# Performance work log

Measured on AMD Instinct MI355X. Metric: run time of the kernel, lower is better.

The kernel has to match this reference:

```python
import jax, jax.numpy as jnp
import numpy as np

RESO = 32          # triplane/voxel resolution
VIT = 16           # ViT patch grid resolution
PAD = 0.1
C_TRI = 64         # triplane channels per plane
C_IMG = 1280       # image feature channels
C_IN = 128         # inner (attention) channels
C_OUT = 64
NH = 8
HD = C_IN // NH
IMG_SIZE = 224.0


def pos_enc(d_model, length):
    pos = jnp.arange(length, dtype=jnp.float32)[:, None]
    div = jnp.exp(jnp.arange(0, d_model, 2, dtype=jnp.float32) * (-np.log(10000.0) / d_model))
    pe = jnp.zeros((length, d_model), jnp.float32)
    pe = pe.at[:, 0::2].set(jnp.sin(pos * div))
    pe = pe.at[:, 1::2].set(jnp.cos(pos * div))
    return pe


def bilinear_sample(feats, gx, gy):
    # feats: [B, J, H, W, C]; gx, gy: [B, J, N] in [-1, 1]; align_corners=True
    B, J, Hh, Ww, _ = feats.shape
    ux = (gx + 1.0) * 0.5 * (Ww - 1)
    uy = (gy + 1.0) * 0.5 * (Hh - 1)
    x0 = jnp.floor(ux).astype(jnp.int32)
    y0 = jnp.floor(uy).astype(jnp.int32)
    wx = (ux - x0)[..., None]
    wy = (uy - y0)[..., None]
    x1 = jnp.clip(x0 + 1, 0, Ww - 1)
    y1 = jnp.clip(y0 + 1, 0, Hh - 1)
    x0 = jnp.clip(x0, 0, Ww - 1)
    y0 = jnp.clip(y0, 0, Hh - 1)
    bi = jnp.arange(B)[:, None, None]
    ji = jnp.arange(J)[None, :, None]
    f00 = feats[bi, ji, y0, x0]
    f01 = feats[bi, ji, y0, x1]
    f10 = feats[bi, ji, y1, x0]
    f11 = feats[bi, ji, y1, x1]
    return (f00 * (1 - wx) * (1 - wy) + f01 * wx * (1 - wy)
            + f10 * (1 - wx) * wy + f11 * wx * wy)


def forward(triplane_feat, image_feat, proj_mat, k_w, k_b, q_w, q_b, v_w, v_b,
            in_w, in_b, out_w, out_b, proj_w, proj_b):
    B, n_img = image_feat.shape[0], image_feat.shape[1]
    N = RESO ** 3
    img = image_feat[:, :, 1:, :]                        # drop CLS -> [B,J,256,C_IMG]
    image_pe = pos_enc(C_IN, VIT * VIT)[None, None]      # [1,1,256,C_IN]
    k_feat = img @ k_w.T + k_b + image_pe
    v_feat = img @ v_w.T + v_b + image_pe
    k_map = k_feat.reshape(B, n_img, VIT, VIT, C_IN)     # [B,J,H,W,C]
    v_map = v_feat.reshape(B, n_img, VIT, VIT, C_IN)

    # voxel coords -> project into each camera
    idx = jnp.arange(RESO)
    X, Y, Z = jnp.meshgrid(idx, idx, idx, indexing='ij')
    vox = jnp.stack([X, Y, Z], -1).reshape(N, 3).astype(jnp.float32)
    vox = (vox / (RESO - 1) - 0.5) * 2.0 * (1.0 + PAD + 1e-5)
    homo = jnp.concatenate([vox, jnp.ones((N, 1), jnp.float32)], -1)  # [N,4]
    pc = jnp.einsum('nk,bjik->bjni', homo, proj_mat)                   # [B,J,N,4]
    px = pc[..., 0] / pc[..., 2]
    py = pc[..., 1] / pc[..., 2]
    gx = jnp.clip((px / (IMG_SIZE - 1) - 0.5) * 2.0, -1.0, 1.0)
    gy = jnp.clip((py / (IMG_SIZE - 1) - 0.5) * 2.0, -1.0, 1.0)
    # The torch code does a 3D grid_sample whose depth coordinate lands exactly
    # on each image index (align_corners=True), so it reduces to per-image
    # bilinear sampling on the 16x16 token maps.
    k_s = bilinear_sample(k_map, gx, gy)   # [B,J,N,C_IN]
    v_s = bilinear_sample(v_map, gx, gy)

    # triplane features expanded to the voxel grid (voxel order n = x*R^2+y*R+z)
    xz, xy, yz = jnp.split(triplane_feat, 3, axis=2)     # each [B,C,R,R]
    xz_t = jnp.transpose(xz, (0, 3, 2, 1))               # [B,x,z,C]
    xy_t = jnp.transpose(xy, (0, 3, 2, 1))               # [B,x,y,C]
    yz_t = jnp.transpose(yz, (0, 3, 2, 1))               # [B,y,z,C]
    shp = (B, RESO, RESO, RESO, C_TRI)
    xz_v = jnp.broadcast_to(xz_t[:, :, None, :, :], shp)
    xy_v = jnp.broadcast_to(xy_t[:, :, :, None, :], shp)
    yz_v = jnp.broadcast_to(yz_t[:, None, :, :, :], shp)
    tri = jnp.concatenate([xz_v, xy_v, yz_v], -1).reshape(B, N, 3 * C_TRI)
    q = tri @ q_w.T + q_b + pos_enc(C_IN, N)[None]       # [B,N,C_IN]

    # per-voxel cross attention (q_len=1, kv_len=n_img); torch MHA semantics
    Wq, Wk, Wv = in_w[:C_IN], in_w[C_IN:2 * C_IN], in_w[2 * C_IN:]
    bq, bk, bv = in_b[:C_IN], in_b[C_IN:2 * C_IN], in_b[2 * C_IN:]
    qh = (q @ Wq.T + bq).reshape(B, N, NH, HD)
    k_t = jnp.transpose(k_s, (0, 2, 1, 3))               # [B,N,J,C]
    v_t = jnp.transpose(v_s, (0, 2, 1, 3))
    kh = (k_t @ Wk.T + bk).reshape(B, N, n_img, NH, HD)
    vh = (v_t @ Wv.T + bv).reshape(B, N, n_img, NH, HD)
    logits = jnp.einsum('bnhd,bnjhd->bnhj', qh, kh) / np.sqrt(HD).astype(np.float32)
    attn = jax.nn.softmax(logits, axis=-1)
    o = jnp.einsum('bnhj,bnjhd->bnhd', attn, vh).reshape(B, N, C_IN)
    o = o @ out_w.T + out_b

    # mean-pool volume back to three planes
    vol = o.reshape(B, RESO, RESO, RESO, C_IN)             # [b,x,y,z,c]
    xz_o = jnp.transpose(vol.mean(axis=2), (0, 2, 1, 3))   # [b,z,x,c]
    xy_o = jnp.transpose(vol.mean(axis=3), (0, 2, 1, 3))   # [b,y,x,c]
    yz_o = jnp.transpose(vol.mean(axis=1), (0, 2, 1, 3))   # [b,z,y,c]
    planes = jnp.concatenate([xz_o, xy_o, yz_o], axis=1)   # [B,3R,R,C_IN]
    out = planes @ proj_w.T + proj_b
    return jnp.transpose(out, (0, 3, 1, 2))                # [B,C_OUT,3R,R]


def setup_inputs() -> dict:
    key = jax.random.key(0)
    ks = jax.random.split(key, 10)
    B, J = 2, 5
    s = 0.02
    base = jnp.array([[200., 0., 112., 0.],
                      [0., 200., 112., 0.],
                      [0., 0., 1., 3.5],
                      [0., 0., 0., 1.]], jnp.float32)
    return {
        'triplane_feat': jax.random.normal(ks[0], (B, C_TRI, 3 * RESO, RESO), jnp.float32),
        'image_feat': jax.random.normal(ks[1], (B, J, VIT * VIT + 1, C_IMG), jnp.float32),
        'proj_mat': base[None, None] + 0.01 * jax.random.normal(ks[2], (B, J, 4, 4), jnp.float32),
        'valid_frames': jnp.ones((B, J), jnp.int32),
        'k_w': s * jax.random.normal(ks[3], (C_IN, C_IMG), jnp.float32), 'k_b': jnp.zeros((C_IN,), jnp.float32),
        'q_w': s * jax.random.normal(ks[4], (C_IN, 3 * C_TRI), jnp.float32), 'q_b': jnp.zeros((C_IN,), jnp.float32),
        'v_w': s * jax.random.normal(ks[5], (C_IN, C_IMG), jnp.float32), 'v_b': jnp.zeros((C_IN,), jnp.float32),
        'in_w': s * jax.random.normal(ks[6], (3 * C_IN, C_IN), jnp.float32), 'in_b': jnp.zeros((3 * C_IN,), jnp.float32),
        'out_w': s * jax.random.normal(ks[7], (C_IN, C_IN), jnp.float32), 'out_b': jnp.zeros((C_IN,), jnp.float32),
        'proj_w': s * jax.random.normal(ks[8], (C_OUT, C_IN), jnp.float32), 'proj_b': jnp.zeros((C_OUT,), jnp.float32),
    }


def reference(triplane_feat, image_feat, proj_mat, valid_frames, k_w, k_b, q_w, q_b,
              v_w, v_b, in_w, in_b, out_w, out_b, proj_w, proj_b):
    # valid_frames matches the torch forward signature but is unused in its body
    return forward(triplane_feat, image_feat, proj_mat, k_w, k_b, q_w, q_b,
                   v_w, v_b, in_w, in_b, out_w, out_b, proj_w, proj_b)
```

## Files before the change

### kernel.cpp

```cpp
#include <hip/hip_runtime.h>
#include <hip/hip_bf16.h>
#include <cstddef>

#define NVOX 32768
#define J5 5
#define KB2 1472
typedef __attribute__((ext_vector_type(8))) short s16x8;
typedef __attribute__((ext_vector_type(8))) _Float16 f16x8;
typedef __attribute__((ext_vector_type(2))) _Float16 h2t;
typedef __attribute__((ext_vector_type(4))) float f32x4;

static __device__ __forceinline__ float pe_val(int pos, int c) {
  float dv = expf((float)(c & ~1) * (-0.0719557841560639f));
  float arg = (float)pos * dv;
  return (c & 1) ? cosf(arg) : sinf(arg);
}
static __device__ __forceinline__ short f2h(float f) {
  _Float16 h = (_Float16)f;
  return *reinterpret_cast<short*>(&h);
}
static __device__ __forceinline__ float h2f(short s) {
  _Float16 h = *reinterpret_cast<_Float16*>(&s);
  return (float)h;
}
static __device__ __forceinline__ float2 cmul(float2 a, float2 b) {
  return make_float2(a.x * b.x - a.y * b.y, a.x * b.y + a.y * b.x);
}
static __device__ __forceinline__ float dot8h(f16x8 a, f16x8 b, float acc) {
#if __has_builtin(__builtin_amdgcn_fdot2)
#pragma unroll
  for (int i = 0; i < 4; i++) {
    h2t x; x[0] = a[2 * i]; x[1] = a[2 * i + 1];
    h2t y; y[0] = b[2 * i]; y[1] = b[2 * i + 1];
    acc = __builtin_amdgcn_fdot2(x, y, acc, false);
  }
#else
#pragma unroll
  for (int i = 0; i < 8; i++) acc = fmaf((float)a[i], (float)b[i], acc);
#endif
  return acc;
}

#define NB_TABS   24
#define NB_WQPE   64
#define NB_WQC    96
#define NB_WO     32
#define NB_QCB    1
#define NB_TRI2   96
#define NB_FOLDW  1280
#define NB_PETAB  128
#define NB_WIN    128
#define NB_CB     1
#define B_TABS   0
#define B_WQPE   (B_TABS + NB_TABS)
#define B_WQC    (B_WQPE + NB_WQPE)
#define B_WO     (B_WQC + NB_WQC)
#define B_QCB    (B_WO + NB_WO)
#define B_TRI2   (B_QCB + NB_QCB)
#define B_FOLDW  (B_TRI2 + NB_TRI2)
#define B_PETAB  (B_FOLDW + NB_FOLDW)
#define B_WIN    (B_PETAB + NB_PETAB)
#define B_CB     (B_WIN + NB_WIN)
#define NB_TOTAL (B_CB + NB_CB)

__global__ __launch_bounds__(256) void k_prep(
    const float* __restrict__ tp,
    const float* __restrict__ k_w, const float* __restrict__ k_b,
    const float* __restrict__ q_w, const float* __restrict__ q_b,
    const float* __restrict__ v_w, const float* __restrict__ v_b,
    const float* __restrict__ in_w, const float* __restrict__ in_b,
    const float* __restrict__ out_w, const float* __restrict__ out_b,
    const float* __restrict__ proj_w, const float* __restrict__ proj_b,
    float2* __restrict__ tabs, short* __restrict__ Wqb_s, float* __restrict__ Wo,
    float* __restrict__ qcb, float* __restrict__ obb,
    short* __restrict__ tri_tb, short* __restrict__ Wkvb2, short* __restrict__ pe_tab) {
  __shared__ short tile_s[64][65];
  const int bx = blockIdx.x, t = threadIdx.x;

  if (bx < B_WQPE) {
    int idx = bx * 256 + t;
    if (idx < 6144) {
      int tb = idx >> 11, rem = idx & 2047;
      int pos = rem >> 6, i = rem & 63;
      float dv = expf((float)(2 * i) * (-0.0719557841560639f));
      float mult = (tb == 0) ? 1024.0f : (tb == 1) ? 32.0f : 1.0f;
      float ang = (float)pos * mult * dv;
      tabs[idx] = make_float2(cosf(ang), sinf(ang));
    }
  } else if (bx < B_WQC) {
    int e = (bx - B_WQPE) * 256 + t;
    int c = e >> 7, j = e & 127;
    Wqb_s[(size_t)c * 320 + 192 + j] = f2h(in_w[(size_t)c * 128 + j]);
  } else if (bx < B_WO) {
    int e = (bx - B_WQC) * 256 + t;
    int c = e / 192, k = e % 192;
    const float* ir = in_w + (size_t)c * 128;
    float acc = 0.f;
    for (int j = 0; j < 128; j++) acc = fmaf(ir[j], q_w[(size_t)j * 192 + k], acc);
    Wqb_s[(size_t)c * 320 + k] = f2h(acc);
  } else if (bx < B_QCB) {
    int e = (bx - B_WO) * 256 + t;
    int o = e >> 7, c = e & 127;
    const float* pr = proj_w + (size_t)o * 128;
    float acc = 0.f;
    for (int j = 0; j < 128; j++) acc = fmaf(pr[j], out_w[(size_t)j * 128 + c], acc);
    Wo[e] = acc;
  } else if (bx < B_TRI2) {
    if (t < 128) {
      float acc = in_b[t];
      const float* ir = in_w + (size_t)t * 128;
      for (int j = 0; j < 128; j++) acc = fmaf(ir[j], q_b[j], acc);
      qcb[t] = acc;
    }
    if (t < 64) {
      float acc = proj_b[t];
      const float* pr = proj_w + (size_t)t * 128;
      for (int j = 0; j < 128; j++) acc = fmaf(pr[j], out_b[j], acc);
      obb[t] = acc;
    }
  } else if (bx < B_FOLDW) {
    int b3 = bx - B_TRI2;
    int segb = b3 >> 4, tile = b3 & 15;
    int b = segb / 3, seg = segb % 3;
    int cc = t >> 2, q = t & 3;
#pragma unroll
    for (int di = 0; di < 2; di++) {
      int i = tile * 2 + di;
      const float* src = tp + (((size_t)(b * 64 + cc)) * 96 + seg * 32 + i) * 32 + q * 8;
      float4 a0 = *(const float4*)src;
      float4 a1 = *(const float4*)(src + 4);
      short* dst = &tile_s[cc][di * 32 + q * 8];
      dst[0] = f2h(a0.x); dst[1] = f2h(a0.y); dst[2] = f2h(a0.z); dst[3] = f2h(a0.w);
      dst[4] = f2h(a1.x); dst[5] = f2h(a1.y); dst[6] = f2h(a1.z); dst[7] = f2h(a1.w);
    }
    __syncthreads();
    int cp = t >> 2;
    int cc0 = q * 16;
    s16x8 v0, v1;
#pragma unroll
    for (int e = 0; e < 8; e++) { v0[e] = tile_s[cc0 + e][cp]; v1[e] = tile_s[cc0 + 8 + e][cp]; }
    short* outp = tri_tb + (((size_t)(b * 3 + seg) * 1024) + tile * 64 + cp) * 64 + cc0;
    *reinterpret_cast<s16x8*>(outp) = v0;
    *reinterpret_cast<s16x8*>(outp + 8) = v1;
  } else if (bx < B_PETAB) {
    int u = (bx - B_FOLDW) * 256 + t;
    int c = u / 1280, k = u % 1280;
    const float* w = (c < 128) ? k_w : v_w;
    const float* ir = in_w + (size_t)(128 + c) * 128;
    float acc = 0.f;
    for (int j = 0; j < 128; j++) acc = fmaf(ir[j], w[(size_t)j * 1280 + k], acc);
    Wkvb2[(size_t)c * KB2 + k] = f2h(acc);
  } else if (bx < B_WIN) {
    int e = (bx - B_PETAB) * 256 + t;
    int p = e >> 7, c = e & 127;
    pe_tab[e] = f2h(pe_val(p, c));
  } else if (bx < B_CB) {
    int e = (bx - B_WIN) * 256 + t;
    int c = e >> 7, j = e & 127;
    Wkvb2[(size_t)c * KB2 + 1280 + j] = f2h(in_w[(size_t)(128 + c) * 128 + j]);
  } else {
    int c = t;
    int which = c >> 7;
    const float* bias = which ? v_b : k_b;
    const float* ir = in_w + (size_t)(128 + c) * 128;
    float acc = in_b[128 + c];
    for (int j = 0; j < 128; j++) acc = fmaf(bias[j], ir[j], acc);
    short* row = Wkvb2 + (size_t)c * KB2 + 1408;
    row[0] = f2h(acc);
    for (int k = 1; k < 64; k++) row[k] = 0;
  }
}

#define NKV 320
__global__ __launch_bounds__(256) void k_qkv(
    const float* __restrict__ img, const short* __restrict__ Wkvb2,
    const short* __restrict__ pe_tab, short* __restrict__ k2b, short* __restrict__ v2b,
    const short* __restrict__ tri_tb, const short* __restrict__ Wqb_s,
    const float* __restrict__ qcb, const float2* __restrict__ tabs,
    short* __restrict__ qh_g) {
  __shared__ __align__(16) short A_lds[64 * 64];
  __shared__ __align__(16) short B_lds[128 * 64];
  const int t = threadIdx.x;
  const int lane = t & 63, w = t >> 6;

  if (blockIdx.x < NKV) {
    const int kvid = blockIdx.x;
    const int m0 = (kvid >> 2) * 32;
    const int nb0 = (kvid & 3) * 64;
    const int wm = w & 1, wn = w >> 1;
    f32x4 acc[2];
    acc[0] = (f32x4){0.f, 0.f, 0.f, 0.f};
    acc[1] = (f32x4){0.f, 0.f, 0.f, 0.f};
    for (int ct = 0; ct < 23; ct++) {
      __syncthreads();
      {
        int r = t >> 3, g = t & 7;
        s16x8 v;
        if (ct < 20) {
          int row = m0 + r;
          int bj = row >> 8, p = row & 255;
          const float* src = img + ((size_t)(bj * 257 + 1 + p)) * 1280 + ct * 64 + g * 8;
          float4 a0 = *(const float4*)src;
          float4 a1 = *(const float4*)(src + 4);
          v[0] = f2h(a0.x); v[1] = f2h(a0.y); v[2] = f2h(a0.z); v[3] = f2h(a0.w);
          v[4] = f2h(a1.x); v[5] = f2h(a1.y); v[6] = f2h(a1.z); v[7] = f2h(a1.w);
        } else if (ct < 22) {
          int p = (m0 + r) & 255;
          v = *reinterpret_cast<const s16x8*>(pe_tab + (size_t)p * 128 + (ct - 20) * 64 + g * 8);
        } else {
          v = (s16x8){0, 0, 0, 0, 0, 0, 0, 0};
          if (g == 0) v[0] = (short)0x3C00;
        }
        *reinterpret_cast<s16x8*>(&A_lds[(r * 8 + (g ^ (r & 7))) * 8]) = v;
      }
      {
#pragma unroll
        for (int it = 0; it < 2; it++) {
          int u = it * 256 + t;
          int r2 = u >> 3, g = u & 7;
          const int4 src = *reinterpret_cast<const int4*>(
              Wkvb2 + (size_t)((kvid & 3) * 64 + r2) * KB2 + ct * 64 + g * 8);
          *reinterpret_cast<int4*>(&B_lds[(r2 * 8 + (g ^ (r2 & 7))) * 8]) = src;
        }
      }
      __syncthreads();
#pragma unroll
      for (int ks = 0; ks < 2; ks++) {
        int kb = ks * 4 + (lane >> 4);
        int arow = wm * 16 + (lane & 15);
        f16x8 a = *reinterpret_cast<const f16x8*>(&A_lds[(arow * 8 + (kb ^ (arow & 7))) * 8]);
#pragma unroll
        for (int f = 0; f < 2; f++) {
          int bcol = wn * 32 + f * 16 + (lane & 15);
          f16x8 bb = *reinterpret_cast<const f16x8*>(&B_lds[(bcol * 8 + (kb ^ (bcol & 7))) * 8]);
          acc[f] = __builtin_amdgcn_mfma_f32_16x16x32_f16(a, bb, acc[f], 0, 0, 0);
        }
      }
    }
#pragma unroll
    for (int f = 0; f < 2; f++) {
#pragma unroll
      for (int reg = 0; reg < 4; reg++) {
        int grow = m0 + wm * 16 + (lane >> 4) * 4 + reg;
        int gcol = nb0 + wn * 32 + f * 16 + (lane & 15);
        int which = gcol >> 7, c = gcol & 127;
        short* dst = which ? v2b : k2b;
        dst[(size_t)grow * 128 + c] = f2h(acc[f][reg]);
      }
    }
  } else {
    const int qid = blockIdx.x - NKV;
    const int b = qid >> 9;
    const int n0 = (qid & 511) * 64;
    const int xq = n0 >> 10, yq0 = (n0 >> 5) & 31;
    const float2* tabX = tabs;
    const float2* tabY = tabs + 2048;
    const float2* tabZ = tabs + 4096;
    f32x4 acc[4][2];
#pragma unroll
    for (int m = 0; m < 4; m++)
#pragma unroll
      for (int f = 0; f < 2; f++) acc[m][f] = (f32x4){0.f, 0.f, 0.f, 0.f};

    for (int ct = 0; ct < 5; ct++) {
      __syncthreads();
      {
#pragma unroll
        for (int it = 0; it < 2; it++) {
          int u = it * 256 + t;
          int r = u >> 3, g = u & 7;
          if (ct < 3) {
            int n = n0 + r;
            int x = n >> 10, y = (n >> 5) & 31, z = n & 31;
            int cell = (ct == 0) ? (z * 32 + x) : (ct == 1) ? (y * 32 + x) : (z * 32 + y);
            const int4 src = *reinterpret_cast<const int4*>(
                tri_tb + ((size_t)(b * 3 + ct) * 1024 + cell) * 64 + g * 8);
            *reinterpret_cast<int4*>(&A_lds[(r * 8 + (g ^ (r & 7))) * 8]) = src;
          } else {
            int i0 = (ct - 3) * 32 + g * 4;
            int z = r & 31, y = yq0 + (r >> 5);
            s16x8 v;
#pragma unroll
            for (int q = 0; q < 4; q++) {
              int i = i0 + q;
              float2 exy = cmul(tabX[xq * 64 + i], tabY[y * 64 + i]);
              float2 e = cmul(exy, tabZ[z * 64 + i]);
              v[q * 2]     = f2h(e.y);
              v[q * 2 + 1] = f2h(e.x);
            }
            *reinterpret_cast<s16x8*>(&A_lds[(r * 8 + (g ^ (r & 7))) * 8]) = v;
          }
        }
      }
      {
#pragma unroll
        for (int it = 0; it < 4; it++) {
          int u = it * 256 + t;
          int col = u >> 3, g = u & 7;
          const int4 src = *reinterpret_cast<const int4*>(
              Wqb_s + (size_t)col * 320 + ct * 64 + g * 8);
          *reinterpret_cast<int4*>(&B_lds[(col * 8 + (g ^ (col & 7))) * 8]) = src;
        }
      }
      __syncthreads();
#pragma unroll
      for (int ks = 0; ks < 2; ks++) {
        int kb = ks * 4 + (lane >> 4);
        f16x8 a[4], bb[2];
#pragma unroll
        for (int m = 0; m < 4; m++) {
          int row = m * 16 + (lane & 15);
          a[m] = *reinterpret_cast<const f16x8*>(&A_lds[(row * 8 + (kb ^ (row & 7))) * 8]);
        }
#pragma unroll
        for (int f = 0; f < 2; f++) {
          int col = w * 32 + f * 16 + (lane & 15);
          bb[f] = *reinterpret_cast<const f16x8*>(&B_lds[(col * 8 + (kb ^ (col & 7))) * 8]);
        }
#pragma unroll
        for (int m = 0; m < 4; m++)
#pragma unroll
          for (int f = 0; f < 2; f++)
            acc[m][f] = __builtin_amdgcn_mfma_f32_16x16x32_f16(a[m], bb[f], acc[m][f], 0, 0, 0);
      }
    }
#pragma unroll
    for (int m = 0; m < 4; m++)
#pragma unroll
      for (int f = 0; f < 2; f++)
#pragma unroll
        for (int reg = 0; reg < 4; reg++) {
          int row = m * 16 + (lane >> 4) * 4 + reg;
          int col = w * 32 + f * 16 + (lane & 15);
          qh_g[((size_t)b * NVOX + n0 + row) * 128 + col] = f2h(acc[m][f][reg] + qcb[col]);
        }
  }
}

__global__ __launch_bounds__(256) void k_attn(
    const short* __restrict__ qh_g, const short* __restrict__ k2b,
    const short* __restrict__ v2b, const float* __restrict__ proj,
    short* __restrict__ obuf, float* __restrict__ pacc) {
  __shared__ __align__(16) ushort sIr[160][4];
  __shared__ __align__(16) float sW4[160][4];
  __shared__ __align__(16) float lg[160 * 8];
  __shared__ __align__(16) short o_lds[32][128];
  __shared__ float sxy[2][128];
  const int b = blockIdx.y;
  const int n0 = blockIdx.x * 32;
  const int t = threadIdx.x;

  if (t < 160) {
    int r = t / J5, j = t % J5;
    int n = n0 + r;
    int x = n >> 10, y = (n >> 5) & 31, z = n & 31;
    const float SC = (float)(1.0 + 0.1 + 1e-05);
    float fx = ((float)x / 31.0f - 0.5f) * 2.0f * SC;
    float fy = ((float)y / 31.0f - 0.5f) * 2.0f * SC;
    float fz = ((float)z / 31.0f - 0.5f) * 2.0f * SC;
    const float* P = proj + (size_t)(b * J5 + j) * 16;
    float pc0 = fmaf(fx, P[0], fmaf(fy, P[1], fmaf(fz, P[2],  P[3])));
    float pc1 = fmaf(fx, P[4], fmaf(fy, P[5], fmaf(fz, P[6],  P[7])));
    float pc2 = fmaf(fx, P[8], fmaf(fy, P[9], fmaf(fz, P[10], P[11])));
    float px = pc0 / pc2, py = pc1 / pc2;
    float gx = fminf(fmaxf((px / 223.0f - 0.5f) * 2.0f, -1.0f), 1.0f);
    float gy = fminf(fmaxf((py / 223.0f - 0.5f) * 2.0f, -1.0f), 1.0f);
    float ux = (gx + 1.0f) * 0.5f * 15.0f;
    float uy = (gy + 1.0f) * 0.5f * 15.0f;
    float fx0 = floorf(ux), fy0 = floorf(uy);
    int x0 = (int)fx0, y0 = (int)fy0;
    float wx = ux - fx0, wy = uy - fy0;
    int x1 = min(x0 + 1, 15), y1 = min(y0 + 1, 15);
    x0 = min(max(x0, 0), 15); y0 = min(max(y0, 0), 15);
    int rowb = (b * J5 + j) * 256;
    sIr[t][0] = (ushort)(rowb + y0 * 16 + x0);
    sIr[t][1] = (ushort)(rowb + y0 * 16 + x1);
    sIr[t][2] = (ushort)(rowb + y1 * 16 + x0);
    sIr[t][3] = (ushort)(rowb + y1 * 16 + x1);
    sW4[t][0] = (1.f - wx) * (1.f - wy);
    sW4[t][1] = wx * (1.f - wy);
    sW4[t][2] = (1.f - wx) * wy;
    sW4[t][3] = wx * wy;
  }
  __syncthreads();

  {
    const int oct = t & 15, rjIdx = t >> 4;
    const int c0 = oct * 8;
#pragma unroll
    for (int it = 0; it < 10; it++) {
      int rj = rjIdx + it * 16;
      int r = rj / J5;
      ushort4 I4 = *reinterpret_cast<const ushort4*>(sIr[rj]);
      float4 W4 = *reinterpret_cast<const float4*>(sW4[rj]);
      f16x8 t0 = *reinterpret_cast<const f16x8*>(k2b + (size_t)I4.x * 128 + c0);
      f16x8 t1 = *reinterpret_cast<const f16x8*>(k2b + (size_t)I4.y * 128 + c0);
      f16x8 t2 = *reinterpret_cast<const f16x8*>(k2b + (size_t)I4.z * 128 + c0);
      f16x8 t3 = *reinterpret_cast<const f16x8*>(k2b + (size_t)I4.w * 128 + c0);
      f16x8 q8 = *reinterpret_cast<const f16x8*>(qh_g + ((size_t)b * NVOX + n0 + r) * 128 + c0);
      float d0 = dot8h(q8, t0, 0.f);
      float d1 = dot8h(q8, t1, 0.f);
      float d2 = dot8h(q8, t2, 0.f);
      float d3 = dot8h(q8, t3, 0.f);
      float pv = fmaf(W4.x, d0, fmaf(W4.y, d1, fmaf(W4.z, d2, W4.w * d3)));
      pv += __shfl_xor(pv, 1);
      if (!(oct & 1)) lg[rj * 8 + (oct >> 1)] = pv * 0.25f;
    }
  }
  __syncthreads();

  {
    int r = t >> 3, h = t & 7;
    float l[J5];
    float m = -1e30f;
#pragma unroll
    for (int j = 0; j < J5; j++) { l[j] = lg[(r * J5 + j) * 8 + h]; m = fmaxf(m, l[j]); }
    float sden = 0.f;
#pragma unroll
    for (int j = 0; j < J5; j++) { l[j] = expf(l[j] - m); sden += l[j]; }
    float inv = 1.0f / sden;
#pragma unroll
    for (int j = 0; j < J5; j++) lg[(r * J5 + j) * 8 + h] = l[j] * inv;
  }
  __syncthreads();

  {
    const int oct = t & 15;
    const int c0 = oct * 8;
#pragma unroll
    for (int it = 0; it < 2; it++) {
      int r = (t >> 4) + it * 16;
      float o8[8] = {0.f, 0.f, 0.f, 0.f, 0.f, 0.f, 0.f, 0.f};
#pragma unroll
      for (int j = 0; j < J5; j++) {
        int rj = r * J5 + j;
        float aw = lg[rj * 8 + (oct >> 1)];
        ushort4 I4 = *reinterpret_cast<const ushort4*>(sIr[rj]);
        float4 W4 = *reinterpret_cast<const float4*>(sW4[rj]);
        float w0 = aw * W4.x, w1 = aw * W4.y, w2 = aw * W4.z, w3 = aw * W4.w;
        f16x8 t0 = *reinterpret_cast<const f16x8*>(v2b + (size_t)I4.x * 128 + c0);
        f16x8 t1 = *reinterpret_cast<const f16x8*>(v2b + (size_t)I4.y * 128 + c0);
        f16x8 t2 = *reinterpret_cast<const f16x8*>(v2b + (size_t)I4.z * 128 + c0);
        f16x8 t3 = *reinterpret_cast<const f16x8*>(v2b + (size_t)I4.w * 128 + c0);
#pragma unroll
        for (int e = 0; e < 8; e++) {
          o8[e] = fmaf(w0, (float)t0[e], o8[e]);
          o8[e] = fmaf(w1, (float)t1[e], o8[e]);
          o8[e] = fmaf(w2, (float)t2[e], o8[e]);
          o8[e] = fmaf(w3, (float)t3[e], o8[e]);
        }
      }
      s16x8 out;
#pragma unroll
      for (int e = 0; e < 8; e++) out[e] = f2h(o8[e]);
      *reinterpret_cast<s16x8*>(obuf + ((size_t)b * NVOX + n0 + r) * 128 + c0) = out;
      *reinterpret_cast<s16x8*>(&o_lds[r][c0]) = out;
    }
  }
  __syncthreads();

  {
    int c = t & 127, half = t >> 7;
    float s = 0.f;
#pragma unroll
    for (int i = 0; i < 16; i++) s += h2f(o_lds[half * 16 + i][c]);
    sxy[half][c] = s;
  }
  __syncthreads();
  if (t < 128) {
    int x = n0 >> 10, y = (n0 >> 5) & 31;
    pacc[((size_t)(b * 96 + 32 + y) * 32 + x) * 128 + t] = sxy[0][t] + sxy[1][t];
  }
}

__global__ __launch_bounds__(128) void k_reduce(const short* __restrict__ obuf,
                                                float* __restrict__ pacc) {
  int blk = blockIdx.x;
  int b = blockIdx.y;
  int t = threadIdx.x;
  int oct = t & 15, sub = t >> 4;
  int c0 = oct * 8;
  int cell = blk * 8 + sub;
  const short* ob = obuf + (size_t)b * NVOX * 128;
  float a8[8] = {0.f, 0.f, 0.f, 0.f, 0.f, 0.f, 0.f, 0.f};
  size_t prow;
  if (cell < 1024) {
    int z = cell >> 5, x = cell & 31;
    for (int y = 0; y < 32; y++) {
      f16x8 u = *reinterpret_cast<const f16x8*>(ob + ((size_t)(x * 1024 + y * 32 + z) * 128 + c0));
#pragma unroll
      for (int e = 0; e < 8; e++) a8[e] += (float)u[e];
    }
    prow = ((size_t)(b * 96 + z) * 32 + x) * 128 + c0;
  } else {
    int e2 = cell - 1024;
    int z = e2 >> 5, y = e2 & 31;
    for (int x = 0; x < 32; x++) {
      f16x8 u = *reinterpret_cast<const f16x8*>(ob + ((size_t)(x * 1024 + y * 32 + z) * 128 + c0));
#pragma unroll
      for (int e = 0; e < 8; e++) a8[e] += (float)u[e];
    }
    prow = ((size_t)(b * 96 + 64 + z) * 32 + y) * 128 + c0;
  }
  *(float4*)(&pacc[prow])     = (float4){a8[0], a8[1], a8[2], a8[3]};
  *(float4*)(&pacc[prow + 4]) = (float4){a8[4], a8[5], a8[6], a8[7]};
}

__global__ __launch_bounds__(128) void k_final(
    const float* __restrict__ pacc, const float* __restrict__ Wo,
    const float* __restrict__ obb, float* __restrict__ outp) {
  int bp = blockIdx.x;
  int b = bp / 96, prow = bp % 96;
  int obase = blockIdx.y * 16;
  __shared__ __align__(16) float lds[32 * 129];
  for (int idx = threadIdx.x; idx < 4096; idx += 128) {
    int col = idx >> 7, k = idx & 127;
    lds[col * 129 + k] = pacc[(size_t)bp * 32 * 128 + idx] * (1.0f / 32.0f);
  }
  __syncthreads();
  for (int e = threadIdx.x; e < 16 * 32; e += 128) {
    int o = obase + (e >> 5), col = e & 31;
    float val = obb[o];
    const float* wr = Wo + (size_t)o * 128;
    const float* lr = lds + col * 129;
    for (int k = 0; k < 128; k++) val = fmaf(wr[k], lr[k], val);
    outp[((size_t)(b * 64 + o) * 96 + prow) * 32 + col] = val;
  }
}

extern "C" void kernel_launch(void* const* d_in, const int* in_sizes, int n_in,
                              void* d_out, int out_size, void* d_ws, size_t ws_size,
                              hipStream_t stream) {
  const float* tp     = (const float*)d_in[0];
  const float* img    = (const float*)d_in[1];
  const float* proj   = (const float*)d_in[2];
  const float* k_w    = (const float*)d_in[4];
  const float* k_b    = (const float*)d_in[5];
  const float* q_w    = (const float*)d_in[6];
  const float* q_b    = (const float*)d_in[7];
  const float* v_w    = (const float*)d_in[8];
  const float* v_b    = (const float*)d_in[9];
  const float* in_w   = (const float*)d_in[10];
  const float* in_b   = (const float*)d_in[11];
  const float* out_w  = (const float*)d_in[12];
  const float* out_b  = (const float*)d_in[13];
  const float* proj_w = (const float*)d_in[14];
  const float* proj_b = (const float*)d_in[15];
  const int B = 2;

  float* ws = (float*)d_ws;
  size_t off = 0;
  short*  tri_tb = (short*)(ws + off);  off += 196608;
  short*  Wkvb2  = (short*)(ws + off);  off += 188416;
  short*  Wqb_s  = (short*)(ws + off);  off += 20480;
  short*  pe_tab = (short*)(ws + off);  off += 16384;
  float2* tabs   = (float2*)(ws + off); off += 12288;
  float*  qcb    = ws + off;            off += 128;
  float*  Wo     = ws + off;            off += 8192;
  float*  obb    = ws + off;            off += 64;
  short*  k2b    = (short*)(ws + off);  off += 163840;
  short*  v2b    = (short*)(ws + off);  off += 163840;
  float*  pacc   = ws + off;            off += 786432;
  short*  qh_g   = (short*)(ws + off);  off += 4194304;
  short*  obuf   = (short*)(ws + off);  off += 2097152;
  if (ws_size < off * sizeof(float)) return;

  k_prep<<<dim3(NB_TOTAL), dim3(256), 0, stream>>>(
      tp, k_w, k_b, q_w, q_b, v_w, v_b, in_w, in_b, out_w, out_b, proj_w, proj_b,
      tabs, Wqb_s, Wo, qcb, obb, tri_tb, Wkvb2, pe_tab);
  k_qkv<<<dim3(NKV + NVOX / 64 * B), dim3(256), 0, stream>>>(
      img, Wkvb2, pe_tab, k2b, v2b, tri_tb, Wqb_s, qcb, tabs, qh_g);
  k_attn<<<dim3(NVOX / 32, B), dim3(256), 0, stream>>>(qh_g, k2b, v2b, proj, obuf, pacc);
  k_reduce<<<dim3(256, B), dim3(128), 0, stream>>>(obuf, pacc);
  k_final<<<dim3(B * 96, 4), dim3(128), 0, stream>>>(pacc, Wo, obb, (float*)d_out);
}
```

Measured before the change: 94.90 us.

## Fuse reduce and final projection, enlarge Q tiles, register-block weight folding

Merges the plane-reduction kernel into the final output projection kernel, so the xz/yz plane sums are computed straight into shared memory instead of round-tripping through pacc. The Q-projection GEMM tile grows from 64 to 128 voxels per block, which reuses each loaded weight tile across more rows at the cost of more accumulator registers and LDS. The weight-folding prep step now computes 8 output channels per thread, reusing each k_w/v_w load across those channels. This removes one launch and reduces redundant global reads, but it lowers block counts and occupancy in the affected kernels.

```diff
diff --git a/kernel.cpp b/kernel.cpp
--- a/kernel.cpp
+++ b/kernel.cpp
@@ -47,7 +47,7 @@
 #define NB_WO     32
 #define NB_QCB    1
 #define NB_TRI2   96
-#define NB_FOLDW  1280
+#define NB_FOLDW  160
 #define NB_PETAB  128
 #define NB_WIN    128
 #define NB_CB     1
@@ -143,13 +143,21 @@
     *reinterpret_cast<s16x8*>(outp) = v0;
     *reinterpret_cast<s16x8*>(outp + 8) = v1;
   } else if (bx < B_PETAB) {
-    int u = (bx - B_FOLDW) * 256 + t;
-    int c = u / 1280, k = u % 1280;
-    const float* w = (c < 128) ? k_w : v_w;
-    const float* ir = in_w + (size_t)(128 + c) * 128;
-    float acc = 0.f;
-    for (int j = 0; j < 128; j++) acc = fmaf(ir[j], w[(size_t)j * 1280 + k], acc);
-    Wkvb2[(size_t)c * KB2 + k] = f2h(acc);
+    int fw = bx - B_FOLDW;
+    int cg = fw / 5, kq = fw % 5;
+    int c0 = cg * 8;
+    int k = kq * 256 + t;
+    const float* w = (c0 < 128) ? k_w : v_w;
+    float acc8[8] = {0, 0, 0, 0, 0, 0, 0, 0};
+    for (int j = 0; j < 128; j++) {
+      float wv = w[(size_t)j * 1280 + k];
+#pragma unroll
+      for (int r = 0; r < 8; r++)
+        acc8[r] = fmaf(in_w[(size_t)(128 + c0 + r) * 128 + j], wv, acc8[r]);
+    }
+#pragma unroll
+    for (int r = 0; r < 8; r++)
+      Wkvb2[(size_t)(c0 + r) * KB2 + k] = f2h(acc8[r]);
   } else if (bx < B_WIN) {
     int e = (bx - B_PETAB) * 256 + t;
     int p = e >> 7, c = e & 127;
@@ -178,7 +186,7 @@
     const short* __restrict__ tri_tb, const short* __restrict__ Wqb_s,
     const float* __restrict__ qcb, const float2* __restrict__ tabs,
     short* __restrict__ qh_g) {
-  __shared__ __align__(16) short A_lds[64 * 64];
+  __shared__ __align__(16) short A_lds[128 * 64];
   __shared__ __align__(16) short B_lds[128 * 64];
   const int t = threadIdx.x;
   const int lane = t & 63, w = t >> 6;
@@ -250,15 +258,15 @@
     }
   } else {
     const int qid = blockIdx.x - NKV;
-    const int b = qid >> 9;
-    const int n0 = (qid & 511) * 64;
+    const int b = qid >> 8;
+    const int n0 = (qid & 255) * 128;
     const int xq = n0 >> 10, yq0 = (n0 >> 5) & 31;
     const float2* tabX = tabs;
     const float2* tabY = tabs + 2048;
     const float2* tabZ = tabs + 4096;
-    f32x4 acc[4][2];
-#pragma unroll
-    for (int m = 0; m < 4; m++)
+    f32x4 acc[8][2];
+#pragma unroll
+    for (int m = 0; m < 8; m++)
 #pragma unroll
       for (int f = 0; f < 2; f++) acc[m][f] = (f32x4){0.f, 0.f, 0.f, 0.f};
 
@@ -266,7 +274,7 @@
       __syncthreads();
       {
 #pragma unroll
-        for (int it = 0; it < 2; it++) {
+        for (int it = 0; it < 4; it++) {
           int u = it * 256 + t;
           int r = u >> 3, g = u & 7;
           if (ct < 3) {
@@ -306,26 +314,24 @@
 #pragma unroll
       for (int ks = 0; ks < 2; ks++) {
         int kb = ks * 4 + (lane >> 4);
-        f16x8 a[4], bb[2];
-#pragma unroll
-        for (int m = 0; m < 4; m++) {
-          int row = m * 16 + (lane & 15);
-          a[m] = *reinterpret_cast<const f16x8*>(&A_lds[(row * 8 + (kb ^ (row & 7))) * 8]);
-        }
+        f16x8 bb[2];
 #pragma unroll
         for (int f = 0; f < 2; f++) {
           int col = w * 32 + f * 16 + (lane & 15);
           bb[f] = *reinterpret_cast<const f16x8*>(&B_lds[(col * 8 + (kb ^ (col & 7))) * 8]);
         }
 #pragma unroll
-        for (int m = 0; m < 4; m++)
+        for (int m = 0; m < 8; m++) {
+          int row = m * 16 + (lane & 15);
+          f16x8 a = *reinterpret_cast<const f16x8*>(&A_lds[(row * 8 + (kb ^ (row & 7))) * 8]);
 #pragma unroll
           for (int f = 0; f < 2; f++)
-            acc[m][f] = __builtin_amdgcn_mfma_f32_16x16x32_f16(a[m], bb[f], acc[m][f], 0, 0, 0);
-      }
-    }
-#pragma unroll
-    for (int m = 0; m < 4; m++)
+            acc[m][f] = __builtin_amdgcn_mfma_f32_16x16x32_f16(a, bb[f], acc[m][f], 0, 0, 0);
+        }
+      }
+    }
+#pragma unroll
+    for (int m = 0; m < 8; m++)
 #pragma unroll
       for (int f = 0; f < 2; f++)
 #pragma unroll
@@ -473,56 +479,48 @@
   }
 }
 
-__global__ __launch_bounds__(128) void k_reduce(const short* __restrict__ obuf,
-                                                float* __restrict__ pacc) {
-  int blk = blockIdx.x;
-  int b = blockIdx.y;
-  int t = threadIdx.x;
-  int oct = t & 15, sub = t >> 4;
-  int c0 = oct * 8;
-  int cell = blk * 8 + sub;
+__global__ __launch_bounds__(256) void k_out(
+    const short* __restrict__ obuf, const float* __restrict__ pacc,
+    const float* __restrict__ Wo, const float* __restrict__ obb,
+    float* __restrict__ outp) {
+  __shared__ __align__(16) float row[32][129];
+  const int bp = blockIdx.x;
+  const int b = bp / 96, prow = bp % 96;
+  const int t = threadIdx.x;
   const short* ob = obuf + (size_t)b * NVOX * 128;
-  float a8[8] = {0.f, 0.f, 0.f, 0.f, 0.f, 0.f, 0.f, 0.f};
-  size_t prow;
-  if (cell < 1024) {
-    int z = cell >> 5, x = cell & 31;
-    for (int y = 0; y < 32; y++) {
-      f16x8 u = *reinterpret_cast<const f16x8*>(ob + ((size_t)(x * 1024 + y * 32 + z) * 128 + c0));
-#pragma unroll
-      for (int e = 0; e < 8; e++) a8[e] += (float)u[e];
-    }
-    prow = ((size_t)(b * 96 + z) * 32 + x) * 128 + c0;
+
+  if (prow < 32 || prow >= 64) {
+    int z = (prow < 32) ? prow : (prow - 64);
+    bool is_xz = (prow < 32);
+    int oct = t & 15, cp = t >> 4;
+    int c0 = oct * 8;
+#pragma unroll
+    for (int ci = 0; ci < 2; ci++) {
+      int cell = cp * 2 + ci;
+      float a8[8] = {0.f, 0.f, 0.f, 0.f, 0.f, 0.f, 0.f, 0.f};
+      for (int m = 0; m < 32; m++) {
+        size_t vox = is_xz ? ((size_t)cell * 1024 + m * 32 + z)
+                           : ((size_t)m * 1024 + cell * 32 + z);
+        f16x8 u = *reinterpret_cast<const f16x8*>(ob + vox * 128 + c0);
+#pragma unroll
+        for (int e = 0; e < 8; e++) a8[e] += (float)u[e];
+      }
+#pragma unroll
+      for (int e = 0; e < 8; e++) row[cell][c0 + e] = a8[e] * (1.0f / 32.0f);
+    }
   } else {
-    int e2 = cell - 1024;
-    int z = e2 >> 5, y = e2 & 31;
-    for (int x = 0; x < 32; x++) {
-      f16x8 u = *reinterpret_cast<const f16x8*>(ob + ((size_t)(x * 1024 + y * 32 + z) * 128 + c0));
-#pragma unroll
-      for (int e = 0; e < 8; e++) a8[e] += (float)u[e];
-    }
-    prow = ((size_t)(b * 96 + 64 + z) * 32 + y) * 128 + c0;
-  }
-  *(float4*)(&pacc[prow])     = (float4){a8[0], a8[1], a8[2], a8[3]};
-  *(float4*)(&pacc[prow + 4]) = (float4){a8[4], a8[5], a8[6], a8[7]};
-}
-
-__global__ __launch_bounds__(128) void k_final(
-    const float* __restrict__ pacc, const float* __restrict__ Wo,
-    const float* __restrict__ obb, float* __restrict__ outp) {
-  int bp = blockIdx.x;
-  int b = bp / 96, prow = bp % 96;
-  int obase = blockIdx.y * 16;
-  __shared__ __align__(16) float lds[32 * 129];
-  for (int idx = threadIdx.x; idx < 4096; idx += 128) {
-    int col = idx >> 7, k = idx & 127;
-    lds[col * 129 + k] = pacc[(size_t)bp * 32 * 128 + idx] * (1.0f / 32.0f);
+    for (int idx = t; idx < 4096; idx += 256) {
+      int col = idx >> 7, k = idx & 127;
+      row[col][k] = pacc[((size_t)(b * 96 + prow) * 32 + col) * 128 + k] * (1.0f / 32.0f);
+    }
   }
   __syncthreads();
-  for (int e = threadIdx.x; e < 16 * 32; e += 128) {
-    int o = obase + (e >> 5), col = e & 31;
+
+  for (int e = t; e < 64 * 32; e += 256) {
+    int o = e >> 5, col = e & 31;
     float val = obb[o];
     const float* wr = Wo + (size_t)o * 128;
-    const float* lr = lds + col * 129;
+    const float* lr = row[col];
     for (int k = 0; k < 128; k++) val = fmaf(wr[k], lr[k], val);
     outp[((size_t)(b * 64 + o) * 96 + prow) * 32 + col] = val;
   }
@@ -568,9 +566,8 @@
   k_prep<<<dim3(NB_TOTAL), dim3(256), 0, stream>>>(
       tp, k_w, k_b, q_w, q_b, v_w, v_b, in_w, in_b, out_w, out_b, proj_w, proj_b,
       tabs, Wqb_s, Wo, qcb, obb, tri_tb, Wkvb2, pe_tab);
-  k_qkv<<<dim3(NKV + NVOX / 64 * B), dim3(256), 0, stream>>>(
+  k_qkv<<<dim3(NKV + NVOX / 128 * B), dim3(256), 0, stream>>>(
       img, Wkvb2, pe_tab, k2b, v2b, tri_tb, Wqb_s, qcb, tabs, qh_g);
   k_attn<<<dim3(NVOX / 32, B), dim3(256), 0, stream>>>(qh_g, k2b, v2b, proj, obuf, pacc);
-  k_reduce<<<dim3(256, B), dim3(128), 0, stream>>>(obuf, pacc);
-  k_final<<<dim3(B * 96, 4), dim3(128), 0, stream>>>(pacc, Wo, obb, (float*)d_out);
-}
+  k_out<<<dim3(B * 96), dim3(256), 0, stream>>>(obuf, pacc, Wo, obb, (float*)d_out);
+}
```

New measurement: 104.6 us. 10.3% more time.
